# Kernel tuning notes

Measured on AMD Instinct MI355X. Metric: run time of the kernel, lower is better.

The kernel has to match this reference:

```python
import jax, jax.numpy as jnp
import numpy as np

N = 20000      # nodes
E = 640000     # edges (before self-loops)
F = 64         # base node feature len
H = 2          # heads per layer
EPS = 1e-5
NEG_SLOPE = 0.2  # PyG GATConv leaky_relu slope


def setup_inputs():
    key = jax.random.key(0)
    ks = jax.random.split(key, 16)
    s = 0.1
    x = jax.random.normal(ks[0], (N, F), jnp.float32)
    edge_index = jax.random.randint(ks[1], (2, E), 0, N, dtype=jnp.int64)
    # layer 1: in=F, heads=H, out-per-head C1=F -> out dim H*F=128
    C1 = F
    W1 = jax.random.normal(ks[2], (F, H * C1), jnp.float32) * s
    att_src1 = jax.random.normal(ks[3], (H, C1), jnp.float32) * s
    att_dst1 = jax.random.normal(ks[4], (H, C1), jnp.float32) * s
    bias1 = jnp.zeros((H * C1,), jnp.float32)
    gamma1 = jnp.ones((H * C1,), jnp.float32)
    beta1 = jnp.zeros((H * C1,), jnp.float32)
    # layer 2: in=H*F=128, heads=H, out-per-head C2=H*F -> out dim H*H*F=256
    C2 = H * F
    W2 = jax.random.normal(ks[5], (H * C1, H * C2), jnp.float32) * s
    att_src2 = jax.random.normal(ks[6], (H, C2), jnp.float32) * s
    att_dst2 = jax.random.normal(ks[7], (H, C2), jnp.float32) * s
    bias2 = jnp.zeros((H * C2,), jnp.float32)
    gamma2 = jnp.ones((H * C2,), jnp.float32)
    beta2 = jnp.zeros((H * C2,), jnp.float32)
    return {"x": x, "edge_index": edge_index,
            "W1": W1, "att_src1": att_src1, "att_dst1": att_dst1, "bias1": bias1,
            "gamma1": gamma1, "beta1": beta1,
            "W2": W2, "att_src2": att_src2, "att_dst2": att_dst2, "bias2": bias2,
            "gamma2": gamma2, "beta2": beta2}


def _gat_conv(x, src, dst, W, att_src, att_dst, bias):
    # PyG GATConv (concat=True, add_self_loops already applied to src/dst)
    n = x.shape[0]
    h, c = att_src.shape
    hx = (x @ W).reshape(n, h, c)                       # [N,H,C]
    a_s = jnp.einsum('nhc,hc->nh', hx, att_src)         # [N,H]
    a_d = jnp.einsum('nhc,hc->nh', hx, att_dst)
    e = a_s[src] + a_d[dst]                             # [E',H]
    e = jnp.where(e > 0, e, NEG_SLOPE * e)              # leaky relu
    # segment softmax over incoming edges of each target node
    m = jax.ops.segment_max(e, dst, num_segments=n)     # [N,H]
    p = jnp.exp(e - m[dst])
    z = jax.ops.segment_sum(p, dst, num_segments=n)     # [N,H]
    alpha = p / z[dst]                                  # [E',H]
    msg = hx[src] * alpha[:, :, None]                   # [E',H,C]
    out = jax.ops.segment_sum(msg, dst, num_segments=n) # [N,H,C]
    return out.reshape(n, h * c) + bias


def _batch_norm(x, gamma, beta):
    mu = x.mean(axis=0)
    var = x.var(axis=0)  # biased, matches torch BN normalization
    return (x - mu) * jax.lax.rsqrt(var + EPS) * gamma + beta


def reference(x, edge_index, W1, att_src1, att_dst1, bias1, gamma1, beta1,
              W2, att_src2, att_dst2, bias2, gamma2, beta2):
    loops = jnp.arange(N, dtype=edge_index.dtype)
    src = jnp.concatenate([edge_index[0], loops])
    dst = jnp.concatenate([edge_index[1], loops])
    h = _gat_conv(x, src, dst, W1, att_src1, att_dst1, bias1)
    h = jax.nn.relu(_batch_norm(h, gamma1, beta1))
    h = _gat_conv(h, src, dst, W2, att_src2, att_dst2, bias2)
    h = jax.nn.relu(_batch_norm(h, gamma2, beta2))
    return h
```

## Files before the change

kernel.cpp:

```cpp
#include <hip/hip_runtime.h>
#include <hip/hip_bf16.h>
#include <math.h>

#define NN 20000
#define ER 640000
#define ET 660000
#define D1 128
#define D2 256
#define EPSV 1e-5f
#define SLOPE 0.2f
#define NT1 313

typedef __attribute__((ext_vector_type(8))) short bf16x8;
typedef __attribute__((ext_vector_type(4))) float f32x4;

__device__ __forceinline__ int detect64(const void* ei) {
  const int* p = (const int*)ei;
  return (p[1] | p[3] | p[5] | p[7]) == 0;
}
__device__ __forceinline__ int clampn(int v) { return v < 0 ? 0 : (v >= NN ? NN-1 : v); }
__device__ __forceinline__ float bf16_lo(unsigned int u){ return __uint_as_float(u<<16); }
__device__ __forceinline__ float bf16_hi(unsigned int u){ return __uint_as_float(u & 0xffff0000u); }

__global__ void k_front(const void* ei, const float* W1, const float* W2,
                        __hip_bfloat16* W1t, __hip_bfloat16* W2c, int* dpart, int* gcount) {
  extern __shared__ int hist[];
  int b = blockIdx.x, t = threadIdx.x;
  if (b == 0 && t == 0) *gcount = 0;
  if (b < 160) {
    int i = b*256 + t;
    if (i < 8192) {
      int n = i >> 6, k = i & 63;
      W1t[i] = __float2bfloat16(W1[k*128 + n]);
    } else {
      int i2 = i - 8192;
      int kc = i2 >> 13, n = (i2 >> 5) & 255, kk = i2 & 31;
      W2c[i2] = __float2bfloat16(W2[(kc*32 + kk)*256 + n]);
    }
    return;
  }
  int db = b - 160;
  for (int i = t; i < NN; i += 256) hist[i] = 0;
  __syncthreads();
  int is64 = detect64(ei);
  int base = db * 80000;
  if (is64) {
    const long long* p64 = (const long long*)ei;
    for (int i = base + t*4; i < base + 80000; i += 1024) {
      uint4 qa = *(const uint4*)(p64 + ER + i);
      uint4 qb = *(const uint4*)(p64 + ER + i + 2);
      atomicAdd(&hist[clampn((int)qa.x)], 1);
      atomicAdd(&hist[clampn((int)qa.z)], 1);
      atomicAdd(&hist[clampn((int)qb.x)], 1);
      atomicAdd(&hist[clampn((int)qb.z)], 1);
    }
  } else {
    const int* p32 = (const int*)ei;
    for (int i = base + t*4; i < base + 80000; i += 1024) {
      uint4 q = *(const uint4*)(p32 + ER + i);
      atomicAdd(&hist[clampn((int)q.x)], 1);
      atomicAdd(&hist[clampn((int)q.y)], 1);
      atomicAdd(&hist[clampn((int)q.z)], 1);
      atomicAdd(&hist[clampn((int)q.w)], 1);
    }
  }
  __syncthreads();
  for (int i = t; i < NN; i += 256) dpart[db*NN + i] = hist[i];
}

__global__ __launch_bounds__(256) void k_alloc(const int* dpart, int* begv, int* endv,
                                               int* cursor, int* gcount, float* bnz) {
  __shared__ int wsum[4], wbase[4];
  int gid = blockIdx.x*256 + threadIdx.x;
  if (gid < 768) bnz[gid] = 0.f;
  int d = 0;
  if (gid < NN) {
    d = 1;
    #pragma unroll
    for (int bb = 0; bb < 8; bb++) d += dpart[bb*NN + gid];
  }
  int lane = threadIdx.x & 63, w = threadIdx.x >> 6;
  int v = d;
  #pragma unroll
  for (int o = 1; o < 64; o <<= 1) {
    int u = __shfl_up(v, o);
    if (lane >= o) v += u;
  }
  if (lane == 63) wsum[w] = v;
  __syncthreads();
  if (threadIdx.x == 0) {
    int s0 = wsum[0], s1 = wsum[1], s2 = wsum[2], s3 = wsum[3];
    int b = atomicAdd(gcount, s0 + s1 + s2 + s3);
    wbase[0] = b; wbase[1] = b + s0; wbase[2] = b + s0 + s1; wbase[3] = b + s0 + s1 + s2;
  }
  __syncthreads();
  if (gid < NN) {
    int beg = wbase[w] + v - d;
    begv[gid] = beg; cursor[gid] = beg; endv[gid] = beg + d;
  }
}

__global__ __launch_bounds__(256) void k_gs(const float* x, const __hip_bfloat16* W1t,
                                            const float* att_s1, const float* att_d1,
                                            __hip_bfloat16* hxb, float2* as1, float2* ad1,
                                            const void* ei, int* cursor, int* srcs) {
  __shared__ __hip_bfloat16 As[64][72];
  __shared__ __hip_bfloat16 Bs[128][72];
  __shared__ float asred[4][64], adred[4][64];
  int b = blockIdx.x, t = threadIdx.x;
  if (b >= NT1) {
    int i0 = ((b - NT1)*256 + t)*4;
    if (i0 >= ET) return;
    int s[4], d[4];
    if (i0 >= ER) {
      #pragma unroll
      for (int k = 0; k < 4; k++) { s[k] = i0 + k - ER; d[k] = s[k]; }
    } else if (detect64(ei)) {
      const long long* p64 = (const long long*)ei;
      uint4 qa = *(const uint4*)(p64 + i0);
      uint4 qb = *(const uint4*)(p64 + i0 + 2);
      uint4 ra = *(const uint4*)(p64 + ER + i0);
      uint4 rb = *(const uint4*)(p64 + ER + i0 + 2);
      s[0]=clampn((int)qa.x); s[1]=clampn((int)qa.z); s[2]=clampn((int)qb.x); s[3]=clampn((int)qb.z);
      d[0]=clampn((int)ra.x); d[1]=clampn((int)ra.z); d[2]=clampn((int)rb.x); d[3]=clampn((int)rb.z);
    } else {
      const int* p32 = (const int*)ei;
      uint4 qs = *(const uint4*)(p32 + i0);
      uint4 qd = *(const uint4*)(p32 + ER + i0);
      s[0]=clampn((int)qs.x); s[1]=clampn((int)qs.y); s[2]=clampn((int)qs.z); s[3]=clampn((int)qs.w);
      d[0]=clampn((int)qd.x); d[1]=clampn((int)qd.y); d[2]=clampn((int)qd.z); d[3]=clampn((int)qd.w);
    }
    #pragma unroll
    for (int k = 0; k < 4; k++) {
      int pos = atomicAdd(&cursor[d[k]], 1);
      srcs[pos] = s[k];
    }
    return;
  }
  int m0 = b * 64;
  for (int i = t; i < 512; i += 256) {
    int r = i >> 3, s = i & 7;
    int gr = m0 + r; if (gr >= NN) gr = NN - 1;
    float4 f0 = ((const float4*)(x + (size_t)gr*64))[s*2];
    float4 f1 = ((const float4*)(x + (size_t)gr*64))[s*2+1];
    __hip_bfloat16 hb[8] = {
      __float2bfloat16(f0.x), __float2bfloat16(f0.y), __float2bfloat16(f0.z), __float2bfloat16(f0.w),
      __float2bfloat16(f1.x), __float2bfloat16(f1.y), __float2bfloat16(f1.z), __float2bfloat16(f1.w)};
    *(uint4*)&As[r][s*8] = *(uint4*)hb;
  }
  for (int i = t; i < 1024; i += 256) {
    int r = i >> 3, s = i & 7;
    *(uint4*)&Bs[r][s*8] = ((const uint4*)(W1t + (size_t)r*64))[s];
  }
  __syncthreads();
  int w = t >> 6, lane = t & 63, lm = lane & 15, q = lane >> 4;
  f32x4 acc[4][2];
  #pragma unroll
  for (int rt = 0; rt < 4; rt++)
    #pragma unroll
    for (int ct = 0; ct < 2; ct++) acc[rt][ct] = (f32x4){0.f,0.f,0.f,0.f};
  #pragma unroll
  for (int kc = 0; kc < 2; kc++) {
    bf16x8 bfr[2];
    #pragma unroll
    for (int ct = 0; ct < 2; ct++)
      bfr[ct] = *(const bf16x8*)&Bs[w*32 + ct*16 + lm][kc*32 + q*8];
    #pragma unroll
    for (int rt = 0; rt < 4; rt++) {
      bf16x8 a = *(const bf16x8*)&As[rt*16 + lm][kc*32 + q*8];
      acc[rt][0] = __builtin_amdgcn_mfma_f32_16x16x32_bf16(a, bfr[0], acc[rt][0], 0, 0, 0);
      acc[rt][1] = __builtin_amdgcn_mfma_f32_16x16x32_bf16(a, bfr[1], acc[rt][1], 0, 0, 0);
    }
  }
  #pragma unroll
  for (int rt = 0; rt < 4; rt++)
    #pragma unroll
    for (int ct = 0; ct < 2; ct++)
      #pragma unroll
      for (int rg = 0; rg < 4; rg++) {
        int row = m0 + rt*16 + q*4 + rg;
        int col = w*32 + ct*16 + lm;
        if (row < NN) hxb[(size_t)row*128 + col] = __float2bfloat16(acc[rt][ct][rg]);
      }
  float asc[2], adc[2];
  #pragma unroll
  for (int ct = 0; ct < 2; ct++) {
    int col = w*32 + ct*16 + lm;
    asc[ct] = att_s1[col]; adc[ct] = att_d1[col];
  }
  #pragma unroll
  for (int rt = 0; rt < 4; rt++)
    #pragma unroll
    for (int rg = 0; rg < 4; rg++) {
      float ps = acc[rt][0][rg]*asc[0] + acc[rt][1][rg]*asc[1];
      float pd = acc[rt][0][rg]*adc[0] + acc[rt][1][rg]*adc[1];
      #pragma unroll
      for (int o = 1; o < 16; o <<= 1) { ps += __shfl_xor(ps, o); pd += __shfl_xor(pd, o); }
      if (lm == 0) { int row = rt*16 + q*4 + rg; asred[w][row] = ps; adred[w][row] = pd; }
    }
  __syncthreads();
  if (t < 64) {
    int row = m0 + t;
    if (row < NN) {
      as1[row] = make_float2(asred[0][t] + asred[1][t], asred[2][t] + asred[3][t]);
      ad1[row] = make_float2(adred[0][t] + adred[1][t], adred[2][t] + adred[3][t]);
    }
  }
}

__global__ __launch_bounds__(256) void k_gemm2f(const float* out1, const __hip_bfloat16* W2c,
                                                const float* bns1, const float* bnq1,
                                                const float* gamma1, const float* beta1,
                                                const float* att_s2, const float* att_d2,
                                                __hip_bfloat16* hxb, float2* as2, float2* ad2) {
  __shared__ __hip_bfloat16 As[64][136];
  __shared__ __hip_bfloat16 Bs[256][40];
  __shared__ float AB[2][128];
  __shared__ float asred[4][64], adred[4][64];
  int t = threadIdx.x;
  int m0 = blockIdx.x * 64;
  if (t < 128) {
    float mean = bns1[t]*(1.f/NN);
    float var  = bnq1[t]*(1.f/NN) - mean*mean;
    float A = rsqrtf(var + EPSV)*gamma1[t];
    AB[0][t] = A; AB[1][t] = beta1[t] - mean*A;
  }
  __syncthreads();
  for (int i = t; i < 1024; i += 256) {
    int r = i >> 4, s = i & 15;
    int gr = m0 + r; if (gr >= NN) gr = NN - 1;
    float4 f0 = ((const float4*)(out1 + (size_t)gr*128))[s*2];
    float4 f1 = ((const float4*)(out1 + (size_t)gr*128))[s*2+1];
    int c = s*8;
    float v[8] = {f0.x,f0.y,f0.z,f0.w,f1.x,f1.y,f1.z,f1.w};
    __hip_bfloat16 hb[8];
    #pragma unroll
    for (int k = 0; k < 8; k++)
      hb[k] = __float2bfloat16(fmaxf(v[k]*AB[0][c+k] + AB[1][c+k], 0.f));
    *(uint4*)&As[r][s*8] = *(uint4*)hb;
  }
  int w = t >> 6, lane = t & 63, lm = lane & 15, q = lane >> 4;
  f32x4 acc[4][4];
  #pragma unroll
  for (int rt = 0; rt < 4; rt++)
    #pragma unroll
    for (int ct = 0; ct < 4; ct++) acc[rt][ct] = (f32x4){0.f,0.f,0.f,0.f};
  for (int kc = 0; kc < 4; kc++) {
    __syncthreads();
    for (int i = t; i < 1024; i += 256) {
      int r = i >> 2, s = i & 3;
      *(uint4*)&Bs[r][s*8] = ((const uint4*)(W2c + ((size_t)kc*256 + r)*32))[s];
    }
    __syncthreads();
    bf16x8 bfr[4];
    #pragma unroll
    for (int ct = 0; ct < 4; ct++)
      bfr[ct] = *(const bf16x8*)&Bs[w*64 + ct*16 + lm][q*8];
    #pragma unroll
    for (int rt = 0; rt < 4; rt++) {
      bf16x8 a = *(const bf16x8*)&As[rt*16 + lm][kc*32 + q*8];
      #pragma unroll
      for (int ct = 0; ct < 4; ct++)
        acc[rt][ct] = __builtin_amdgcn_mfma_f32_16x16x32_bf16(a, bfr[ct], acc[rt][ct], 0, 0, 0);
    }
  }
  #pragma unroll
  for (int rt = 0; rt < 4; rt++)
    #pragma unroll
    for (int ct = 0; ct < 4; ct++)
      #pragma unroll
      for (int rg = 0; rg < 4; rg++) {
        int row = m0 + rt*16 + q*4 + rg;
        int col = w*64 + ct*16 + lm;
        if (row < NN) hxb[(size_t)row*256 + col] = __float2bfloat16(acc[rt][ct][rg]);
      }
  float asc[4], adc[4];
  #pragma unroll
  for (int ct = 0; ct < 4; ct++) {
    int col = w*64 + ct*16 + lm;
    asc[ct] = att_s2[col]; adc[ct] = att_d2[col];
  }
  #pragma unroll
  for (int rt = 0; rt < 4; rt++)
    #pragma unroll
    for (int rg = 0; rg < 4; rg++) {
      float ps = acc[rt][0][rg]*asc[0] + acc[rt][1][rg]*asc[1]
               + acc[rt][2][rg]*asc[2] + acc[rt][3][rg]*asc[3];
      float pd = acc[rt][0][rg]*adc[0] + acc[rt][1][rg]*adc[1]
               + acc[rt][2][rg]*adc[2] + acc[rt][3][rg]*adc[3];
      #pragma unroll
      for (int o = 1; o < 16; o <<= 1) { ps += __shfl_xor(ps, o); pd += __shfl_xor(pd, o); }
      if (lm == 0) { int row = rt*16 + q*4 + rg; asred[w][row] = ps; adred[w][row] = pd; }
    }
  __syncthreads();
  if (t < 64) {
    int row = m0 + t;
    if (row < NN) {
      as2[row] = make_float2(asred[0][t] + asred[1][t], asred[2][t] + asred[3][t]);
      ad2[row] = make_float2(adred[0][t] + adred[1][t], adred[2][t] + adred[3][t]);
    }
  }
}

__global__ __launch_bounds__(64) void k_agg1(const int* begv, const int* endv, const int* srcs,
                                             const float2* asv, const float2* adv,
                                             const uint4* hx, const float* bias, float* out) {
  __shared__ float2 sp[2][64];
  int n = blockIdx.x, t = threadIdx.x;
  int el = t >> 4, c = t & 15;
  int h = c >> 3;
  float2 ad = adv[n];
  int beg = begv[n], end = endv[n];
  float a[8] = {0.f,0.f,0.f,0.f,0.f,0.f,0.f,0.f};
  float z0 = 0.f, z1 = 0.f;
  for (int cb = beg; cb < end; cb += 64) {
    int len = end - cb; if (len > 64) len = 64;
    if (t < len) {
      int s = srcs[cb + t];
      float2 as = asv[s];
      float e0 = as.x + ad.x, e1 = as.y + ad.y;
      e0 = e0 > 0.f ? e0 : SLOPE*e0;
      e1 = e1 > 0.f ? e1 : SLOPE*e1;
      float p0 = __expf(e0), p1 = __expf(e1);
      sp[0][t] = make_float2(__int_as_float(s), p0);
      sp[1][t] = make_float2(__int_as_float(s), p1);
      z0 += p0; z1 += p1;
    }
    __syncthreads();
    for (int j = 0; j < len; j += 4) {
      int e = j + el;
      if (e < len) {
        float2 v = sp[h][e];
        uint4 u = hx[(size_t)__float_as_int(v.x)*16 + c];
        float pj = v.y;
        a[0] += pj*bf16_lo(u.x); a[1] += pj*bf16_hi(u.x);
        a[2] += pj*bf16_lo(u.y); a[3] += pj*bf16_hi(u.y);
        a[4] += pj*bf16_lo(u.z); a[5] += pj*bf16_hi(u.z);
        a[6] += pj*bf16_lo(u.w); a[7] += pj*bf16_hi(u.w);
      }
    }
    __syncthreads();
  }
  #pragma unroll
  for (int k = 0; k < 8; k++) {
    a[k] += __shfl_down(a[k], 32);
    a[k] += __shfl_down(a[k], 16);
  }
  #pragma unroll
  for (int o = 1; o < 64; o <<= 1) { z0 += __shfl_xor(z0, o); z1 += __shfl_xor(z1, o); }
  if (t < 16) {
    float inv = 1.f / (h ? z1 : z0);
    float4 b0 = ((const float4*)bias)[2*c];
    float4 b1 = ((const float4*)bias)[2*c+1];
    float4 o0 = { a[0]*inv + b0.x, a[1]*inv + b0.y, a[2]*inv + b0.z, a[3]*inv + b0.w };
    float4 o1 = { a[4]*inv + b1.x, a[5]*inv + b1.y, a[6]*inv + b1.z, a[7]*inv + b1.w };
    ((float4*)(out + (size_t)n*D1))[2*c]   = o0;
    ((float4*)(out + (size_t)n*D1))[2*c+1] = o1;
  }
}

__global__ __launch_bounds__(64) void k_agg2(const int* begv, const int* endv, const int* srcs,
                                             const float2* asv, const float2* adv,
                                             const uint4* hx, const float* bias, float* out) {
  __shared__ float2 sp[2][64];
  int n = blockIdx.x, t = threadIdx.x;
  int el = t >> 5, c = t & 31;
  int h = c >> 4;
  float2 ad = adv[n];
  int beg = begv[n], end = endv[n];
  float a[8] = {0.f,0.f,0.f,0.f,0.f,0.f,0.f,0.f};
  float z0 = 0.f, z1 = 0.f;
  for (int cb = beg; cb < end; cb += 64) {
    int len = end - cb; if (len > 64) len = 64;
    if (t < len) {
      int s = srcs[cb + t];
      float2 as = asv[s];
      float e0 = as.x + ad.x, e1 = as.y + ad.y;
      e0 = e0 > 0.f ? e0 : SLOPE*e0;
      e1 = e1 > 0.f ? e1 : SLOPE*e1;
      float p0 = __expf(e0), p1 = __expf(e1);
      sp[0][t] = make_float2(__int_as_float(s), p0);
      sp[1][t] = make_float2(__int_as_float(s), p1);
      z0 += p0; z1 += p1;
    }
    __syncthreads();
    for (int j = 0; j < len; j += 2) {
      int e = j + el;
      if (e < len) {
        float2 v = sp[h][e];
        uint4 u = hx[(size_t)__float_as_int(v.x)*32 + c];
        float pj = v.y;
        a[0] += pj*bf16_lo(u.x); a[1] += pj*bf16_hi(u.x);
        a[2] += pj*bf16_lo(u.y); a[3] += pj*bf16_hi(u.y);
        a[4] += pj*bf16_lo(u.z); a[5] += pj*bf16_hi(u.z);
        a[6] += pj*bf16_lo(u.w); a[7] += pj*bf16_hi(u.w);
      }
    }
    __syncthreads();
  }
  #pragma unroll
  for (int k = 0; k < 8; k++) a[k] += __shfl_down(a[k], 32);
  #pragma unroll
  for (int o = 1; o < 64; o <<= 1) { z0 += __shfl_xor(z0, o); z1 += __shfl_xor(z1, o); }
  if (t < 32) {
    float inv = 1.f / (h ? z1 : z0);
    float4 b0 = ((const float4*)bias)[2*c];
    float4 b1 = ((const float4*)bias)[2*c+1];
    float4 o0 = { a[0]*inv + b0.x, a[1]*inv + b0.y, a[2]*inv + b0.z, a[3]*inv + b0.w };
    float4 o1 = { a[4]*inv + b1.x, a[5]*inv + b1.y, a[6]*inv + b1.z, a[7]*inv + b1.w };
    ((float4*)(out + (size_t)n*D2))[2*c]   = o0;
    ((float4*)(out + (size_t)n*D2))[2*c+1] = o1;
  }
}

template<int D>
__global__ void k_bnstats(const float* x, float* bnsum, float* bnsq) {
  const int ROWS = 100;
  int c = threadIdx.x;
  int r0 = blockIdx.x * ROWS;
  float s = 0.f, s2 = 0.f;
  for (int r = 0; r < ROWS; r++) {
    float v = x[(size_t)(r0 + r)*D + c];
    s += v; s2 += v*v;
  }
  atomicAdd(&bnsum[c], s);
  atomicAdd(&bnsq[c], s2);
}

__global__ void k_bnapply2(const float* x, const float* bnsum, const float* bnsq,
                           const float* gamma, const float* beta, float* out) {
  int i = blockIdx.x*blockDim.x + threadIdx.x;
  if (i >= NN*D2/4) return;
  int c = (i & 63) * 4;
  float4 v = ((const float4*)x)[i];
  float r[4] = {v.x, v.y, v.z, v.w};
  #pragma unroll
  for (int k = 0; k < 4; k++) {
    float mean = bnsum[c+k] * (1.f/NN);
    float var  = bnsq[c+k] * (1.f/NN) - mean*mean;
    float o = (r[k] - mean) * rsqrtf(var + EPSV) * gamma[c+k] + beta[c+k];
    r[k] = o > 0.f ? o : 0.f;
  }
  float4 o4 = {r[0], r[1], r[2], r[3]};
  ((float4*)out)[i] = o4;
}

extern "C" void kernel_launch(void* const* d_in, const int* in_sizes, int n_in,
                              void* d_out, int out_size, void* d_ws, size_t ws_size,
                              hipStream_t stream) {
  const float* x      = (const float*)d_in[0];
  const void*  ei     = d_in[1];
  const float* W1     = (const float*)d_in[2];
  const float* att_s1 = (const float*)d_in[3];
  const float* att_d1 = (const float*)d_in[4];
  const float* bias1  = (const float*)d_in[5];
  const float* gamma1 = (const float*)d_in[6];
  const float* beta1  = (const float*)d_in[7];
  const float* W2     = (const float*)d_in[8];
  const float* att_s2 = (const float*)d_in[9];
  const float* att_d2 = (const float*)d_in[10];
  const float* bias2  = (const float*)d_in[11];
  const float* gamma2 = (const float*)d_in[12];
  const float* beta2  = (const float*)d_in[13];

  char* p = (char*)d_ws;
  __hip_bfloat16* hx1b = (__hip_bfloat16*)p; p += (size_t)NN*D1*2;
  __hip_bfloat16* hx2b = (__hip_bfloat16*)p; p += (size_t)NN*D2*2;
  __hip_bfloat16* W1t  = (__hip_bfloat16*)p; p += 8192*2;
  __hip_bfloat16* W2c  = (__hip_bfloat16*)p; p += 32768*2;
  float* out1 = (float*)p; p += (size_t)NN*D1*4;
  float* out2 = (float*)p; p += (size_t)NN*D2*4;
  float2* as1 = (float2*)p; p += (size_t)NN*8;
  float2* ad1 = (float2*)p; p += (size_t)NN*8;
  float2* as2 = (float2*)p; p += (size_t)NN*8;
  float2* ad2 = (float2*)p; p += (size_t)NN*8;
  float* bns1 = (float*)p; p += D1*4;
  float* bnq1 = (float*)p; p += D1*4;
  float* bns2 = (float*)p; p += D2*4;
  float* bnq2 = (float*)p; p += D2*4;
  int* dpart  = (int*)p; p += (size_t)8*NN*4;
  int* begv   = (int*)p; p += NN*4;
  int* endv   = (int*)p; p += NN*4;
  int* cursor = (int*)p; p += NN*4;
  int* gcount = (int*)p; p += 16*4;
  int* srcs   = (int*)p; p += (size_t)ET*4;

  const int SCB = (ET/4 + 255)/256;
  k_front<<<168, 256, NN*sizeof(int), stream>>>(ei, W1, W2, W1t, W2c, dpart, gcount);
  k_alloc<<<(NN+255)/256, 256, 0, stream>>>(dpart, begv, endv, cursor, gcount, bns1);
  k_gs<<<NT1 + SCB, 256, 0, stream>>>(x, W1t, att_s1, att_d1, hx1b, as1, ad1,
                                      ei, cursor, srcs);

  k_agg1<<<NN, 64, 0, stream>>>(begv, endv, srcs, as1, ad1, (const uint4*)hx1b, bias1, out1);
  k_bnstats<D1><<<200, D1, 0, stream>>>(out1, bns1, bnq1);

  k_gemm2f<<<(NN+63)/64, 256, 0, stream>>>(out1, W2c, bns1, bnq1, gamma1, beta1,
                                           att_s2, att_d2, hx2b, as2, ad2);
  k_agg2<<<NN, 64, 0, stream>>>(begv, endv, srcs, as2, ad2, (const uint4*)hx2b, bias2, out2);
  k_bnstats<D2><<<200, D2, 0, stream>>>(out2, bns2, bnq2);
  k_bnapply2<<<(NN*D2/4 + 255)/256, 256, 0, stream>>>(out2, bns2, bnq2, gamma2, beta2,
                                                      (float*)d_out);
}
```

Measured before the change: 260.4 us.

## Split degree histogram into 64 chunked blocks and convert weights inside GEMM kernels

The degree histogram now runs across 64 blocks of 10000 edges each instead of 8 blocks of 80000. Each block packs two 16-bit counters per shared-memory word, so a full-node histogram fits in less LDS. k_alloc then sums 64 partials per node. The separate weight transpose/bf16 conversion pass is removed, and each GEMM block converts W1/W2 from fp32 directly into shared memory. This trades extra per-block scalar strided global loads and more partial-sum reads for more histogram parallelism and one less preprocessing step.

```diff
diff --git a/kernel.cpp b/kernel.cpp
--- a/kernel.cpp
+++ b/kernel.cpp
@@ -10,6 +10,8 @@
 #define EPSV 1e-5f
 #define SLOPE 0.2f
 #define NT1 313
+#define NHIST 64
+#define HCH 10000
 
 typedef __attribute__((ext_vector_type(8))) short bf16x8;
 typedef __attribute__((ext_vector_type(4))) float f32x4;
@@ -22,53 +24,31 @@
 __device__ __forceinline__ float bf16_lo(unsigned int u){ return __uint_as_float(u<<16); }
 __device__ __forceinline__ float bf16_hi(unsigned int u){ return __uint_as_float(u & 0xffff0000u); }
 
-__global__ void k_front(const void* ei, const float* W1, const float* W2,
-                        __hip_bfloat16* W1t, __hip_bfloat16* W2c, int* dpart, int* gcount) {
-  extern __shared__ int hist[];
-  int b = blockIdx.x, t = threadIdx.x;
-  if (b == 0 && t == 0) *gcount = 0;
-  if (b < 160) {
-    int i = b*256 + t;
-    if (i < 8192) {
-      int n = i >> 6, k = i & 63;
-      W1t[i] = __float2bfloat16(W1[k*128 + n]);
-    } else {
-      int i2 = i - 8192;
-      int kc = i2 >> 13, n = (i2 >> 5) & 255, kk = i2 & 31;
-      W2c[i2] = __float2bfloat16(W2[(kc*32 + kk)*256 + n]);
-    }
-    return;
-  }
-  int db = b - 160;
-  for (int i = t; i < NN; i += 256) hist[i] = 0;
-  __syncthreads();
-  int is64 = detect64(ei);
-  int base = db * 80000;
-  if (is64) {
-    const long long* p64 = (const long long*)ei;
-    for (int i = base + t*4; i < base + 80000; i += 1024) {
-      uint4 qa = *(const uint4*)(p64 + ER + i);
-      uint4 qb = *(const uint4*)(p64 + ER + i + 2);
-      atomicAdd(&hist[clampn((int)qa.x)], 1);
-      atomicAdd(&hist[clampn((int)qa.z)], 1);
-      atomicAdd(&hist[clampn((int)qb.x)], 1);
-      atomicAdd(&hist[clampn((int)qb.z)], 1);
+__global__ void k_hist(const void* ei, unsigned int* dpart, int* gcount) {
+  extern __shared__ unsigned int hist[];
+  int db = blockIdx.x, t = threadIdx.x;
+  if (db == 0 && t == 0) *gcount = 0;
+  for (int i = t; i < HCH; i += 256) hist[i] = 0;
+  __syncthreads();
+  int base = db * HCH;
+  if (detect64(ei)) {
+    const long long* q = (const long long*)ei + ER;
+    for (int i = base + t; i < base + HCH; i += 256) {
+      int d = clampn((int)q[i]);
+      atomicAdd(&hist[d>>1], 1u << ((d&1)*16));
     }
   } else {
-    const int* p32 = (const int*)ei;
-    for (int i = base + t*4; i < base + 80000; i += 1024) {
-      uint4 q = *(const uint4*)(p32 + ER + i);
-      atomicAdd(&hist[clampn((int)q.x)], 1);
-      atomicAdd(&hist[clampn((int)q.y)], 1);
-      atomicAdd(&hist[clampn((int)q.z)], 1);
-      atomicAdd(&hist[clampn((int)q.w)], 1);
-    }
-  }
-  __syncthreads();
-  for (int i = t; i < NN; i += 256) dpart[db*NN + i] = hist[i];
-}
-
-__global__ __launch_bounds__(256) void k_alloc(const int* dpart, int* begv, int* endv,
+    const int* q = (const int*)ei + ER;
+    for (int i = base + t; i < base + HCH; i += 256) {
+      int d = clampn(q[i]);
+      atomicAdd(&hist[d>>1], 1u << ((d&1)*16));
+    }
+  }
+  __syncthreads();
+  for (int i = t; i < HCH; i += 256) dpart[(size_t)db*HCH + i] = hist[i];
+}
+
+__global__ __launch_bounds__(256) void k_alloc(const unsigned int* dpart, int* begv, int* endv,
                                                int* cursor, int* gcount, float* bnz) {
   __shared__ int wsum[4], wbase[4];
   int gid = blockIdx.x*256 + threadIdx.x;
@@ -76,8 +56,10 @@
   int d = 0;
   if (gid < NN) {
     d = 1;
-    #pragma unroll
-    for (int bb = 0; bb < 8; bb++) d += dpart[bb*NN + gid];
+    int half = (gid & 1) * 16;
+    int idx = gid >> 1;
+    for (int db = 0; db < NHIST; db++)
+      d += (dpart[(size_t)db*HCH + idx] >> half) & 0xffff;
   }
   int lane = threadIdx.x & 63, w = threadIdx.x >> 6;
   int v = d;
@@ -100,7 +82,7 @@
   }
 }
 
-__global__ __launch_bounds__(256) void k_gs(const float* x, const __hip_bfloat16* W1t,
+__global__ __launch_bounds__(256) void k_gs(const float* x, const float* W1,
                                             const float* att_s1, const float* att_d1,
                                             __hip_bfloat16* hxb, float2* as1, float2* ad1,
                                             const void* ei, int* cursor, int* srcs) {
@@ -148,9 +130,9 @@
       __float2bfloat16(f1.x), __float2bfloat16(f1.y), __float2bfloat16(f1.z), __float2bfloat16(f1.w)};
     *(uint4*)&As[r][s*8] = *(uint4*)hb;
   }
-  for (int i = t; i < 1024; i += 256) {
-    int r = i >> 3, s = i & 7;
-    *(uint4*)&Bs[r][s*8] = ((const uint4*)(W1t + (size_t)r*64))[s];
+  for (int i = t; i < 8192; i += 256) {
+    int n = i & 127, k = i >> 7;
+    Bs[n][k] = __float2bfloat16(W1[k*128 + n]);
   }
   __syncthreads();
   int w = t >> 6, lane = t & 63, lm = lane & 15, q = lane >> 4;
@@ -208,7 +190,7 @@
   }
 }
 
-__global__ __launch_bounds__(256) void k_gemm2f(const float* out1, const __hip_bfloat16* W2c,
+__global__ __launch_bounds__(256) void k_gemm2f(const float* out1, const float* W2,
                                                 const float* bns1, const float* bnq1,
                                                 const float* gamma1, const float* beta1,
                                                 const float* att_s2, const float* att_d2,
@@ -247,9 +229,9 @@
     for (int ct = 0; ct < 4; ct++) acc[rt][ct] = (f32x4){0.f,0.f,0.f,0.f};
   for (int kc = 0; kc < 4; kc++) {
     __syncthreads();
-    for (int i = t; i < 1024; i += 256) {
-      int r = i >> 2, s = i & 3;
-      *(uint4*)&Bs[r][s*8] = ((const uint4*)(W2c + ((size_t)kc*256 + r)*32))[s];
+    for (int i = t; i < 8192; i += 256) {
+      int n = i & 255, kk = i >> 8;
+      Bs[n][kk] = __float2bfloat16(W2[(kc*32 + kk)*256 + n]);
     }
     __syncthreads();
     bf16x8 bfr[4];
@@ -466,8 +448,6 @@
   char* p = (char*)d_ws;
   __hip_bfloat16* hx1b = (__hip_bfloat16*)p; p += (size_t)NN*D1*2;
   __hip_bfloat16* hx2b = (__hip_bfloat16*)p; p += (size_t)NN*D2*2;
-  __hip_bfloat16* W1t  = (__hip_bfloat16*)p; p += 8192*2;
-  __hip_bfloat16* W2c  = (__hip_bfloat16*)p; p += 32768*2;
   float* out1 = (float*)p; p += (size_t)NN*D1*4;
   float* out2 = (float*)p; p += (size_t)NN*D2*4;
   float2* as1 = (float2*)p; p += (size_t)NN*8;
@@ -478,7 +458,7 @@
   float* bnq1 = (float*)p; p += D1*4;
   float* bns2 = (float*)p; p += D2*4;
   float* bnq2 = (float*)p; p += D2*4;
-  int* dpart  = (int*)p; p += (size_t)8*NN*4;
+  unsigned int* dpart = (unsigned int*)p; p += (size_t)NHIST*HCH*4;
   int* begv   = (int*)p; p += NN*4;
   int* endv   = (int*)p; p += NN*4;
   int* cursor = (int*)p; p += NN*4;
@@ -486,15 +466,15 @@
   int* srcs   = (int*)p; p += (size_t)ET*4;
 
   const int SCB = (ET/4 + 255)/256;
-  k_front<<<168, 256, NN*sizeof(int), stream>>>(ei, W1, W2, W1t, W2c, dpart, gcount);
+  k_hist<<<NHIST, 256, HCH*4, stream>>>(ei, dpart, gcount);
   k_alloc<<<(NN+255)/256, 256, 0, stream>>>(dpart, begv, endv, cursor, gcount, bns1);
-  k_gs<<<NT1 + SCB, 256, 0, stream>>>(x, W1t, att_s1, att_d1, hx1b, as1, ad1,
+  k_gs<<<NT1 + SCB, 256, 0, stream>>>(x, W1, att_s1, att_d1, hx1b, as1, ad1,
                                       ei, cursor, srcs);
 
   k_agg1<<<NN, 64, 0, stream>>>(begv, endv, srcs, as1, ad1, (const uint4*)hx1b, bias1, out1);
   k_bnstats<D1><<<200, D1, 0, stream>>>(out1, bns1, bnq1);
 
-  k_gemm2f<<<(NN+63)/64, 256, 0, stream>>>(out1, W2c, bns1, bnq1, gamma1, beta1,
+  k_gemm2f<<<(NN+63)/64, 256, 0, stream>>>(out1, W2, bns1, bnq1, gamma1, beta1,
                                            att_s2, att_d2, hx2b, as2, ad2);
   k_agg2<<<NN, 64, 0, stream>>>(begv, endv, srcs, as2, ad2, (const uint4*)hx2b, bias2, out2);
   k_bnstats<D2><<<200, D2, 0, stream>>>(out2, bns2, bnq2);
```

Result: faster. 254.3 us (median of 3 runs) (-2.3%).
